# Kernel optimization log

Hardware: AMD Instinct MI355X
Metric: run time of the kernel (lower is better)

Reference implementation:

```python
import jax, jax.numpy as jnp
import numpy as np

DIM = 128
HEADS = 4
KV_RANK = 64
Q_RANK = 32
ROPE = DIM // 2   # 64
NOPE = DIM // 2   # 64
VDIM = DIM // 2   # 64
B, H, W = 2, 64, 64
EPS = 1e-5


def _conv1x1(x, w, b):
    # x: [B,C,H,W], w: [O,C], b: [O]
    return jnp.einsum('bchw,oc->bohw', x, w) + b[None, :, None, None]


def _gn1(x, g, b):
    # GroupNorm with 1 group: normalize over (C,H,W) per sample
    mu = jnp.mean(x, axis=(1, 2, 3), keepdims=True)
    var = jnp.mean((x - mu) ** 2, axis=(1, 2, 3), keepdims=True)
    return (x - mu) / jnp.sqrt(var + EPS) * g[None, :, None, None] + b[None, :, None, None]


def _freqs(h, w):
    # Replicates RotaryPositionalEncoding: pe[...,0::4]=sin_h, 1::4=cos_h, 2::4=sin_w, 3::4=cos_w
    n = ROPE // 4
    inv = 1.0 / (10000.0 ** (jnp.arange(n, dtype=jnp.float32) / n))
    ah = jnp.arange(h, dtype=jnp.float32)[:, None] * inv  # [h,n]
    aw = jnp.arange(w, dtype=jnp.float32)[:, None] * inv  # [w,n]
    fh = jnp.stack([jnp.sin(ah), jnp.cos(ah)], -1)  # [h,n,2] -> (real=sin_h, imag=cos_h)
    fw = jnp.stack([jnp.sin(aw), jnp.cos(aw)], -1)  # [w,n,2]
    fh_b = jnp.broadcast_to(fh[:, None], (h, w, n, 2))
    fw_b = jnp.broadcast_to(fw[None, :], (h, w, n, 2))
    # interleave pairs: pair 2m -> fh[m], pair 2m+1 -> fw[m]
    pe = jnp.stack([fh_b, fw_b], axis=3).reshape(h * w, ROPE // 2, 2)
    return pe  # [S, ROPE//2, 2]


def _rope(x, f):
    # x: [..., S, ROPE]; f: [S, ROPE//2, 2]
    xp = x.reshape(x.shape[:-1] + (ROPE // 2, 2))
    fr, fi = f[..., 0], f[..., 1]  # [S, ROPE//2] broadcast over leading dims
    rr = xp[..., 0] * fr - xp[..., 1] * fi
    ri = xp[..., 0] * fi + xp[..., 1] * fr
    return jnp.stack([rr, ri], -1).reshape(x.shape)


def setup_inputs() -> dict:
    key = jax.random.key(0)
    ks = jax.random.split(key, 8)
    s = 0.02
    inp = {
        'x': jax.random.normal(ks[0], (B, DIM, H, W), dtype=jnp.float32),
        'q1_w': jax.random.normal(ks[1], (Q_RANK, DIM), dtype=jnp.float32) * s,
        'q1_b': jnp.zeros((Q_RANK,), jnp.float32),
        'q_gn_g': jnp.ones((Q_RANK,), jnp.float32),
        'q_gn_b': jnp.zeros((Q_RANK,), jnp.float32),
        'q2_w': jax.random.normal(ks[2], (HEADS * (NOPE + ROPE), Q_RANK), dtype=jnp.float32) * s,
        'q2_b': jnp.zeros((HEADS * (NOPE + ROPE),), jnp.float32),
        'kv1_w': jax.random.normal(ks[3], (KV_RANK + ROPE, DIM), dtype=jnp.float32) * s,
        'kv1_b': jnp.zeros((KV_RANK + ROPE,), jnp.float32),
        'kv_gn_g': jnp.ones((KV_RANK + ROPE,), jnp.float32),
        'kv_gn_b': jnp.zeros((KV_RANK + ROPE,), jnp.float32),
        'kvn_g': jnp.ones((KV_RANK,), jnp.float32),
        'kvn_b': jnp.zeros((KV_RANK,), jnp.float32),
        'kvup_w': jax.random.normal(ks[4], (HEADS * (NOPE + VDIM), KV_RANK), dtype=jnp.float32) * s,
        'kvup_b': jnp.zeros((HEADS * (NOPE + VDIM),), jnp.float32),
        'out_w': jax.random.normal(ks[5], (DIM, HEADS * VDIM), dtype=jnp.float32) * s,
        'out_b': jnp.zeros((DIM,), jnp.float32),
    }
    return inp


def reference(x, q1_w, q1_b, q_gn_g, q_gn_b, q2_w, q2_b, kv1_w, kv1_b, kv_gn_g, kv_gn_b, kvn_g, kvn_b, kvup_w, kvup_b, out_w, out_b):
    b, c, h, w = x.shape
    s = h * w
    f = _freqs(h, w)  # [S, ROPE//2, 2]

    # Q path: low-rank down -> GN -> up
    q = _conv1x1(_gn1(_conv1x1(x, q1_w, q1_b), q_gn_g, q_gn_b), q2_w, q2_b)
    q = q.reshape(b, HEADS, NOPE + ROPE, s).transpose(0, 1, 3, 2)  # [B,H,S,D]
    q_nope, q_rope = q[..., :NOPE], q[..., NOPE:]
    q = jnp.concatenate([q_nope, _rope(q_rope, f)], axis=-1)

    # KV path: joint down-proj, split rope-k and compressed kv
    kv = _gn1(_conv1x1(x, kv1_w, kv1_b), kv_gn_g, kv_gn_b)  # [B, ROPE+KV_RANK, H, W]
    k_rope_c, kv_c = kv[:, :ROPE], kv[:, ROPE:]
    kv_u = _conv1x1(_gn1(kv_c, kvn_g, kvn_b), kvup_w, kvup_b)
    kv_u = kv_u.reshape(b, HEADS, NOPE + VDIM, s).transpose(0, 1, 3, 2)
    k_nope, v = kv_u[..., :NOPE], kv_u[..., NOPE:]

    k_rope = _rope(k_rope_c.reshape(b, ROPE, s).transpose(0, 2, 1)[:, None], f)  # [B,1,S,ROPE]
    k = jnp.concatenate([k_nope, jnp.broadcast_to(k_rope, (b, HEADS, s, ROPE))], axis=-1)

    scale = (NOPE + ROPE) ** -0.5
    attn = jax.nn.softmax(jnp.einsum('bhqd,bhkd->bhqk', q, k) * scale, axis=-1)
    o = jnp.einsum('bhqk,bhkd->bhqd', attn, v)  # [B,H,S,VDIM]
    o = o.transpose(0, 1, 3, 2).reshape(b, HEADS * VDIM, h, w)
    return _conv1x1(o, out_w, out_b) + x
```

## Files before the change

### kernel.cpp

```cpp
#include <hip/hip_runtime.h>

typedef unsigned short ushort_t;
typedef unsigned int uint_t;
typedef __attribute__((ext_vector_type(8))) short s16x8;
typedef __attribute__((ext_vector_type(4))) short s16x4;
typedef __attribute__((ext_vector_type(4))) float f32x4;
typedef __attribute__((ext_vector_type(16))) float f32x16;

#define S_TOT 4096
#define QSCALE 0.08838834764831845f
#define LOG2E 1.4426950408889634f
#define QSL (QSCALE * LOG2E)
#define L2_10000_D16 0.8304820237218406f

__device__ __forceinline__ ushort_t f2b(float f) {
  uint_t u = __float_as_uint(f);
  uint_t r = (u + 0x7FFFu + ((u >> 16) & 1u)) >> 16;
  return (ushort_t)r;
}

__device__ __forceinline__ float b2f(ushort_t u) {
  return __uint_as_float((uint_t)u << 16);
}

__device__ __forceinline__ uint_t cvt_pk_bf16(float lo, float hi) {
  uint_t r;
  asm("v_cvt_pk_bf16_f32 %0, %1, %2" : "=v"(r) : "v"(lo), "v"(hi));
  return r;
}

__device__ __forceinline__ void gload16(const void* g, void* l) {
  __builtin_amdgcn_global_load_lds(
      (const __attribute__((address_space(1))) unsigned int*)g,
      (__attribute__((address_space(3))) unsigned int*)l, 16, 0, 0);
}

__device__ __forceinline__ void rope_pair_t(float& x0, float& x1, int p, int hi, int wi,
                                            float scale, const float2* __restrict__ tab) {
  int j = p >> 1;
  int src = (p & 1) ? wi : hi;
  float2 sc = tab[src * 16 + j];
  float r0 = (x0 * sc.x - x1 * sc.y) * scale;
  float r1 = (x0 * sc.y + x1 * sc.x) * scale;
  x0 = r0; x1 = r1;
}

__global__ __launch_bounds__(256) void k_conv1(
    const float* __restrict__ x, const float* __restrict__ q1_w, const float* __restrict__ q1_b,
    const float* __restrict__ kv1_w, const float* __restrict__ kv1_b,
    float* __restrict__ y_q, float* __restrict__ y_kv, double* __restrict__ pch,
    const float* __restrict__ q2_w, const float* __restrict__ q2_b,
    const float* __restrict__ kvup_w, const float* __restrict__ kvup_b,
    const float* __restrict__ out_w, const float* __restrict__ out_b,
    ushort_t* __restrict__ wq2, ushort_t* __restrict__ wout,
    float* __restrict__ q2b2, float* __restrict__ outb2) {
  if (blockIdx.x >= 512) {
    int E = (blockIdx.x - 512) * 256 + threadIdx.x;
    if (E < 16384) {
      int oc = E >> 5, r = E & 31;
      int h = oc >> 7, d = oc & 127;
      float val;
      if (d < 64) {
        val = 0.f;
        for (int dd = 0; dd < 64; dd++)
          val += kvup_w[(h * 128 + dd) * 64 + d] * q2_w[(size_t)(h * 128 + dd) * 32 + r];
      } else {
        val = q2_w[(size_t)oc * 32 + r];
      }
      wq2[(size_t)oc * 32 + r] = f2b(val);
    } else if (E < 49152) {
      int e = E - 16384;
      int c = e >> 8, col = e & 255;
      int h = col >> 6, l = col & 63;
      float val = 0.f;
      for (int vd = 0; vd < 64; vd++)
        val += out_w[(size_t)c * 256 + h * 64 + vd] * kvup_w[(h * 128 + 64 + vd) * 64 + l];
      wout[(size_t)c * 256 + col] = f2b(val);
    } else if (E < 49664) {
      int oc = E - 49152;
      int h = oc >> 7, d = oc & 127;
      float val;
      if (d < 64) {
        val = 0.f;
        for (int dd = 0; dd < 64; dd++)
          val += kvup_w[(h * 128 + dd) * 64 + d] * q2_b[h * 128 + dd];
      } else val = q2_b[oc];
      q2b2[oc] = val;
    } else if (E < 49792) {
      int c = E - 49664;
      float val = out_b[c];
      for (int j = 0; j < 256; j++) {
        int h = j >> 6, vd = j & 63;
        val += out_w[(size_t)c * 256 + j] * kvup_b[h * 128 + 64 + vd];
      }
      outb2[c] = val;
    }
    return;
  }
  const int b = blockIdx.x >> 8, blk = blockIdx.x & 255, st = blk * 16;
  const int t = threadIdx.x, si = t & 15, g = t >> 4;
  __shared__ float xs[128][16];
#pragma unroll
  for (int i = 0; i < 8; i++) {
    int c = g + 16 * i;
    xs[c][si] = x[(size_t)(b * 128 + c) * S_TOT + st + si];
  }
  __syncthreads();
  float acc[10];
#pragma unroll
  for (int i = 0; i < 10; i++) {
    int oc = g * 10 + i;
    acc[i] = (oc < 32) ? q1_b[oc] : kv1_b[oc - 32];
  }
  const float4* q1w4 = (const float4*)q1_w;
  const float4* kv1w4 = (const float4*)kv1_w;
  for (int c4 = 0; c4 < 32; c4++) {
    float x0 = xs[c4 * 4 + 0][si], x1 = xs[c4 * 4 + 1][si];
    float x2 = xs[c4 * 4 + 2][si], x3 = xs[c4 * 4 + 3][si];
#pragma unroll
    for (int i = 0; i < 10; i++) {
      int oc = g * 10 + i;
      float4 wv = (oc < 32) ? q1w4[oc * 32 + c4] : kv1w4[(oc - 32) * 32 + c4];
      acc[i] += wv.x * x0 + wv.y * x1 + wv.z * x2 + wv.w * x3;
    }
  }
#pragma unroll
  for (int i = 0; i < 10; i++) {
    int oc = g * 10 + i;
    float a = acc[i];
    if (oc < 32) y_q[(size_t)(b * 32 + oc) * S_TOT + st + si] = a;
    else         y_kv[(size_t)(b * 128 + oc - 32) * S_TOT + st + si] = a;
    double s = a, q = (double)a * a;
#pragma unroll
    for (int o = 1; o < 16; o <<= 1) { s += __shfl_xor(s, o, 16); q += __shfl_xor(q, o, 16); }
    if (si == 0) {
      double* pt = pch + (size_t)(b * 160 + oc) * 512 + blk * 2;
      pt[0] = s; pt[1] = q;
    }
  }
}

__global__ __launch_bounds__(256) void k_red(
    const double* __restrict__ pch, double* __restrict__ SQ) {
  const int pair = blockIdx.x, tid = threadIdx.x;
  const int lane = tid & 63, wid = tid >> 6;
  const double* p = pch + (size_t)pair * 512;
  double s = p[tid * 2], q = p[tid * 2 + 1];
#pragma unroll
  for (int o = 1; o < 64; o <<= 1) { s += __shfl_xor(s, o, 64); q += __shfl_xor(q, o, 64); }
  __shared__ double red[4][2];
  if (lane == 0) { red[wid][0] = s; red[wid][1] = q; }
  __syncthreads();
  if (tid == 0) {
    SQ[pair * 2]     = red[0][0] + red[1][0] + red[2][0] + red[3][0];
    SQ[pair * 2 + 1] = red[0][1] + red[1][1] + red[2][1] + red[3][1];
  }
}

__global__ __launch_bounds__(512) void k_stats(
    const double* __restrict__ SQ,
    const float* __restrict__ qg, const float* __restrict__ qb,
    const float* __restrict__ kvg, const float* __restrict__ kvb,
    const float* __restrict__ kng, const float* __restrict__ knb,
    float* __restrict__ coef, float2* __restrict__ tab) {
  __shared__ double Sh[2][160], Qh[2][160];
  const int tid = threadIdx.x;
  for (int i = tid; i < 1024; i += 512) {
    int src = i >> 4, j = i & 15;
    float inv = exp2f(-(float)j * L2_10000_D16);
    float ang = (float)src * inv;
    tab[i] = make_float2(sinf(ang), cosf(ang));
  }
  if (tid < 320) {
    int b = tid / 160, c = tid % 160;
    Sh[b][c] = SQ[tid * 2]; Qh[b][c] = SQ[tid * 2 + 1];
  }
  __syncthreads();
  if (tid < 2) {
    int b = tid;
    float* cf = coef + b * 320;
    const double NS = 4096.0;
    double muq = 0, m2q = 0;
    for (int c = 0; c < 32; c++) { muq += Sh[b][c]; m2q += Qh[b][c]; }
    muq /= (32.0 * NS); m2q /= (32.0 * NS);
    double rstdq = 1.0 / sqrt(m2q - muq * muq + 1e-5);
    for (int c = 0; c < 32; c++) {
      double A = rstdq * (double)qg[c];
      cf[c] = (float)A; cf[32 + c] = (float)((double)qb[c] - muq * A);
    }
    double mukv = 0, m2kv = 0;
    for (int c = 0; c < 128; c++) { mukv += Sh[b][32 + c]; m2kv += Qh[b][32 + c]; }
    mukv /= (128.0 * NS); m2kv /= (128.0 * NS);
    double rstdkv = 1.0 / sqrt(m2kv - mukv * mukv + 1e-5);
    for (int c = 0; c < 64; c++) {
      double A = rstdkv * (double)kvg[c];
      cf[64 + c] = (float)A; cf[128 + c] = (float)((double)kvb[c] - mukv * A);
    }
    double mu2 = 0, m22 = 0;
    for (int c2 = 0; c2 < 64; c2++) {
      int c = 64 + c2;
      double a = rstdkv * (double)kvg[c], bb = (double)kvb[c] - mukv * a;
      double Ec = Sh[b][32 + c] / NS, M2c = Qh[b][32 + c] / NS;
      mu2 += a * Ec + bb;
      m22 += a * a * M2c + 2.0 * a * bb * Ec + bb * bb;
    }
    mu2 /= 64.0; m22 /= 64.0;
    double rstd2 = 1.0 / sqrt(m22 - mu2 * mu2 + 1e-5);
    for (int c2 = 0; c2 < 64; c2++) {
      int c = 64 + c2;
      double a = rstdkv * (double)kvg[c], bb = (double)kvb[c] - mukv * a;
      cf[192 + c2] = (float)(a * rstd2 * (double)kng[c2]);
      cf[256 + c2] = (float)((bb - mu2) * rstd2 * (double)kng[c2] + (double)knb[c2]);
    }
  }
}

__device__ __forceinline__ void gq_body(
    int id, ushort_t* smem,
    const float* __restrict__ y_q, const float* __restrict__ coef,
    const ushort_t* __restrict__ wq2, const float* __restrict__ q2b2,
    const float2* __restrict__ tab, ushort_t* __restrict__ Q) {
  const int h = id & 3, st = (id >> 2) & 63, b = id >> 8;
  const int t = threadIdx.x, si = t & 63, wid = t >> 6;
  const int l15 = t & 15, lg = (t >> 4) & 3;
  const float* cf = coef + b * 320;
  ushort_t* Xt = smem;
  ushort_t* sQ = smem + 4096;
  {
    ushort_t pk[8];
#pragma unroll
    for (int j = 0; j < 8; j++) {
      int c = wid * 8 + j;
      float v = y_q[(size_t)(b * 32 + c) * S_TOT + st * 64 + si];
      pk[j] = f2b(v * cf[c] + cf[32 + c]);
    }
    *(s16x8*)((char*)(Xt + si * 64) + ((wid * 16) ^ ((si & 7) << 4))) = *(s16x8*)pk;
  }
  __syncthreads();
  const int d0w = wid * 32;
  f32x4 acc[2][4];
#pragma unroll
  for (int db = 0; db < 2; db++) {
    f32x4 bv;
#pragma unroll
    for (int r = 0; r < 4; r++) bv[r] = q2b2[h * 128 + d0w + db * 16 + lg * 4 + r];
#pragma unroll
    for (int sb = 0; sb < 4; sb++) acc[db][sb] = bv;
  }
  s16x8 wf[2];
#pragma unroll
  for (int db = 0; db < 2; db++)
    wf[db] = *(const s16x8*)(wq2 + (size_t)(h * 128 + d0w + db * 16 + l15) * 32 + lg * 8);
  const int xsw = (lg * 16) ^ ((l15 & 7) << 4);
#pragma unroll
  for (int sb = 0; sb < 4; sb++) {
    s16x8 xf = *(const s16x8*)((const char*)(Xt + (sb * 16 + l15) * 64) + xsw);
#pragma unroll
    for (int db = 0; db < 2; db++)
      acc[db][sb] = __builtin_amdgcn_mfma_f32_16x16x32_bf16(wf[db], xf, acc[db][sb], 0, 0, 0);
  }
  if (wid >= 2) {
#pragma unroll
    for (int db = 0; db < 2; db++)
#pragma unroll
      for (int sb = 0; sb < 4; sb++) {
        int sp = st * 64 + sb * 16 + l15, hi = sp >> 6, wi = sp & 63;
        int dg = d0w + db * 16 + lg * 4;
#pragma unroll
        for (int pr = 0; pr < 2; pr++) {
          float v0 = acc[db][sb][pr * 2], v1 = acc[db][sb][pr * 2 + 1];
          int p = (dg + pr * 2 - 64) >> 1;
          rope_pair_t(v0, v1, p, hi, wi, QSL, tab);
          acc[db][sb][pr * 2] = v0; acc[db][sb][pr * 2 + 1] = v1;
        }
      }
  } else {
#pragma unroll
    for (int db = 0; db < 2; db++)
#pragma unroll
      for (int sb = 0; sb < 4; sb++)
#pragma unroll
        for (int r = 0; r < 4; r++) acc[db][sb][r] *= QSL;
  }
#pragma unroll
  for (int db = 0; db < 2; db++)
#pragma unroll
    for (int sb = 0; sb < 4; sb++) {
      ushort_t pk[4];
#pragma unroll
      for (int r = 0; r < 4; r++) pk[r] = f2b(acc[db][sb][r]);
      int srow = sb * 16 + l15;
      *(s16x4*)((char*)(sQ + srow * 128) + (((d0w + db * 16 + lg * 4) * 2) ^ ((srow & 7) << 4))) =
          *(s16x4*)pk;
    }
  __syncthreads();
  ushort_t* qrow = Q + ((size_t)(b * 4 + h) * S_TOT + st * 64 + si) * 128 + wid * 32;
#pragma unroll
  for (int j = 0; j < 4; j++) {
    s16x8 v = *(const s16x8*)((const char*)(sQ + si * 128) + ((wid * 64 + j * 16) ^ ((si & 7) << 4)));
    *(s16x8*)(qrow + j * 8) = v;
  }
}

__device__ __forceinline__ void lat_body(
    int blk, const float* __restrict__ y_kv, const float* __restrict__ coef,
    const float2* __restrict__ tab, ushort_t* __restrict__ C, ushort_t* __restrict__ VT) {
  const int b = blk >> 6, st = (blk & 63) * 64;
  const int t = threadIdx.x, si = t & 63, g = t >> 6;
  const float* cf = coef + b * 320;
  const int sp = st + si;
  if (g < 2) {
    const int c0 = g * 32;
    float v[32];
#pragma unroll
    for (int j = 0; j < 32; j++) {
      int c = c0 + j;
      v[j] = y_kv[(size_t)(b * 128 + c) * S_TOT + sp] * cf[64 + c] + cf[128 + c];
    }
    const int hi = sp >> 6, wi = sp & 63;
#pragma unroll
    for (int k = 0; k < 16; k++)
      rope_pair_t(v[2 * k], v[2 * k + 1], (c0 >> 1) + k, hi, wi, 1.0f, tab);
    ushort_t pk[32];
#pragma unroll
    for (int j = 0; j < 32; j++) pk[j] = f2b(v[j]);
    ushort_t* crow = C + (size_t)(b * S_TOT + sp) * 128 + 64 + c0;
#pragma unroll
    for (int j4 = 0; j4 < 4; j4++) *(s16x8*)(crow + j4 * 8) = *(s16x8*)(pk + j4 * 8);
  } else {
    const int c0 = (g - 2) * 32;
    ushort_t pk[32];
#pragma unroll
    for (int j = 0; j < 32; j++) {
      int c2 = c0 + j;
      float v = y_kv[(size_t)(b * 128 + 64 + c2) * S_TOT + sp] * cf[192 + c2] + cf[256 + c2];
      ushort_t u = f2b(v);
      pk[j] = u;
      VT[(size_t)(b * 64 + c2) * S_TOT + sp] = u;
    }
    ushort_t* crow = C + (size_t)(b * S_TOT + sp) * 128 + c0;
#pragma unroll
    for (int j4 = 0; j4 < 4; j4++) *(s16x8*)(crow + j4 * 8) = *(s16x8*)(pk + j4 * 8);
  }
}

__global__ __launch_bounds__(256) void k_build(
    const float* __restrict__ y_q, const float* __restrict__ y_kv,
    const float* __restrict__ coef,
    const ushort_t* __restrict__ wq2, const float* __restrict__ q2b2,
    const float2* __restrict__ tab,
    ushort_t* __restrict__ Q, ushort_t* __restrict__ C, ushort_t* __restrict__ VT) {
  __shared__ __align__(16) ushort_t smem[12288];
  if (blockIdx.x < 512) gq_body(blockIdx.x, smem, y_q, coef, wq2, q2b2, tab, Q);
  else                  lat_body(blockIdx.x - 512, y_kv, coef, tab, C, VT);
}

__global__ __launch_bounds__(256, 2) void k_attn(
    const ushort_t* __restrict__ Q, const ushort_t* __restrict__ C,
    const ushort_t* __restrict__ VT, ushort_t* __restrict__ Opart,
    float* __restrict__ lvec) {
  const int bid = blockIdx.x;
  const int bh = bid & 7;
  const int rest = bid >> 3;
  const int half = rest >> 5, qblk = rest & 31;
  const int kv0 = half * 2048;
  const int tid = threadIdx.x;
  const int wid = tid >> 6, lane = tid & 63;
  const int l31 = lane & 31, hi = lane >> 5;
  const int qbase = qblk * 128 + wid * 32;
  const int b4 = bh >> 2;
  const ushort_t* Qp = Q + (size_t)bh * S_TOT * 128;
  const ushort_t* Kp = C + (size_t)b4 * S_TOT * 128;
  const ushort_t* Vp = VT + (size_t)b4 * 64 * S_TOT;

  __shared__ __align__(16) ushort_t K_lds[3][64][128];
  __shared__ __align__(16) ushort_t V_lds[3][64][64];

  s16x8 qf[8];
#pragma unroll
  for (int c = 0; c < 8; c++)
    qf[c] = *(const s16x8*)(Qp + (size_t)(qbase + l31) * 128 + c * 16 + hi * 8);

  f32x16 o0, o1;
#pragma unroll
  for (int r = 0; r < 16; r++) { o0[r] = 0.f; o1[r] = 0.f; }
  float l_s = 0.f;

  const int krow_l = tid >> 4;
  const int kcolb = (tid & 15) * 16;
  const int vrow_l = tid >> 3;
  const int vcolb = (tid & 7) * 16;

#define STAGE(kvb, bufi)                                                          \
  {                                                                               \
    _Pragma("unroll")                                                             \
    for (int i = 0; i < 4; i++) {                                                 \
      int row = i * 16 + krow_l;                                                  \
      int colb = kcolb ^ ((row & 15) << 4);                                       \
      gload16((const char*)(Kp + (size_t)((kvb) + row) * 128) + colb,             \
              (void*)&K_lds[bufi][i * 16 + wid * 4][0]);                          \
    }                                                                             \
    _Pragma("unroll")                                                             \
    for (int i = 0; i < 2; i++) {                                                 \
      int vd = i * 32 + vrow_l;                                                   \
      int colb = vcolb ^ ((vd & 7) << 4);                                         \
      gload16((const char*)(Vp + (size_t)vd * S_TOT + (kvb)) + colb,              \
              (void*)&V_lds[bufi][i * 32 + wid * 8][0]);                          \
    }                                                                             \
  }

  STAGE(kv0, 0);
  STAGE(kv0 + 64, 1);

  const int kswz = (l31 & 15) << 4;
  const int vswz = (l31 & 7) << 4;
#pragma unroll 1
  for (int t = 0; t < 32; t++) {
    const int buf = t % 3;
    if (t < 31) {
      asm volatile("s_waitcnt vmcnt(6)" ::: "memory");
    } else {
      asm volatile("s_waitcnt vmcnt(0)" ::: "memory");
    }
    __builtin_amdgcn_sched_barrier(0);
    __builtin_amdgcn_s_barrier();
    __builtin_amdgcn_sched_barrier(0);
    if (t < 30) STAGE(kv0 + (t + 2) * 64, (t + 2) % 3);
    f32x16 sc0, sc1;
#pragma unroll
    for (int r = 0; r < 16; r++) { sc0[r] = 0.f; sc1[r] = 0.f; }
    __builtin_amdgcn_s_setprio(1);
#pragma unroll
    for (int c = 0; c < 8; c++) {
      const int off = (c * 32 + hi * 16) ^ kswz;
      s16x8 k0 = *(const s16x8*)((const char*)&K_lds[buf][l31][0] + off);
      s16x8 k1 = *(const s16x8*)((const char*)&K_lds[buf][32 + l31][0] + off);
      sc0 = __builtin_amdgcn_mfma_f32_32x32x16_bf16(k0, qf[c], sc0, 0, 0, 0);
      sc1 = __builtin_amdgcn_mfma_f32_32x32x16_bf16(k1, qf[c], sc1, 0, 0, 0);
    }
    __builtin_amdgcn_s_setprio(0);
    float rs = 0.f;
#pragma unroll
    for (int r = 0; r < 16; r++) {
      float p0 = exp2f(sc0[r]);
      float p1 = exp2f(sc1[r]);
      sc0[r] = p0; sc1[r] = p1;
      rs += p0 + p1;
    }
    l_s += rs;
    __builtin_amdgcn_s_setprio(1);
#pragma unroll
    for (int c = 0; c < 4; c++) {
      const f32x16 P = (c < 2) ? sc0 : sc1;
      const int rA = 8 * (c & 1);
      uint_t a0 = cvt_pk_bf16(P[rA + 0], P[rA + 1]);
      uint_t a1 = cvt_pk_bf16(P[rA + 2], P[rA + 3]);
      uint_t b0 = cvt_pk_bf16(P[rA + 4], P[rA + 5]);
      uint_t b1 = cvt_pk_bf16(P[rA + 6], P[rA + 7]);
      asm volatile("v_permlane32_swap_b32 %0, %1" : "+v"(a0), "+v"(b0));
      asm volatile("v_permlane32_swap_b32 %0, %1" : "+v"(a1), "+v"(b1));
      union { uint_t u[4]; s16x8 v; } pf;
      pf.u[0] = a0; pf.u[1] = a1;
      pf.u[2] = b0; pf.u[3] = b1;
      const int voff = (c * 32 + hi * 16) ^ vswz;
      s16x8 v0 = *(const s16x8*)((const char*)&V_lds[buf][l31][0] + voff);
      s16x8 v1 = *(const s16x8*)((const char*)&V_lds[buf][32 + l31][0] + voff);
      o0 = __builtin_amdgcn_mfma_f32_32x32x16_bf16(v0, pf.v, o0, 0, 0, 0);
      o1 = __builtin_amdgcn_mfma_f32_32x32x16_bf16(v1, pf.v, o1, 0, 0, 0);
    }
    __builtin_amdgcn_s_setprio(0);
  }
#undef STAGE
  l_s += __shfl_xor(l_s, 32, 64);
  if (lane < 32)
    lvec[((size_t)(half * 8 + bh) << 12) + qbase + l31] = l_s;
  char* sO = (char*)&K_lds[0][0][0];
#pragma unroll
  for (int vt = 0; vt < 2; vt++) {
#pragma unroll
    for (int r = 0; r < 16; r += 2) {
      float v0 = (vt ? o1[r] : o0[r]);
      float v1 = (vt ? o1[r + 1] : o0[r + 1]);
      uint_t u = cvt_pk_bf16(v0, v1);
      int vd = vt * 32 + (r & 3) + 8 * (r >> 2) + 4 * hi;
      *(uint_t*)(sO + (wid * 32 + l31) * 128 + ((vd * 2) ^ ((l31 & 7) << 4))) = u;
    }
  }
  __syncthreads();
  {
    const int r = tid >> 1, hf = tid & 1;
    const int w = r >> 5, ql = r & 31;
    ushort_t* orow = Opart + ((size_t)(half * 8 + bh) * S_TOT + qblk * 128 + r) * 64 + hf * 32;
#pragma unroll
    for (int j = 0; j < 4; j++) {
      s16x8 v = *(const s16x8*)(sO + (w * 32 + ql) * 128 + ((hf * 64 + j * 16) ^ ((ql & 7) << 4)));
      *(s16x8*)(orow + j * 8) = v;
    }
  }
}

__global__ __launch_bounds__(256) void k_oc(
    const ushort_t* __restrict__ Opart, const float* __restrict__ lvec,
    const ushort_t* __restrict__ wout, const float* __restrict__ outb2,
    const float* __restrict__ x, float* __restrict__ out) {
  const int id = blockIdx.x;
  const int cch = id & 1, st32 = (id >> 1) & 127, b = id >> 8;
  const int t = threadIdx.x, wid = t >> 6;
  const int l15 = t & 15, lg = (t >> 4) & 3;
  __shared__ __align__(16) ushort_t Xt[32][256];
  {
    const int s = t & 31, grp = t >> 5;
    const int h = grp >> 1, vd0 = (grp & 1) * 32;
    const int sp = st32 * 32 + s;
    const float l0 = lvec[((size_t)(b * 4 + h) << 12) + sp];
    const float l1 = lvec[((size_t)(8 + b * 4 + h) << 12) + sp];
    const float w = 1.f / (l0 + l1);
    const ushort_t* oa = Opart + ((size_t)(b * 4 + h) * S_TOT + sp) * 64 + vd0;
    const ushort_t* obp = oa + (size_t)8 * S_TOT * 64;
#pragma unroll
    for (int j4 = 0; j4 < 4; j4++) {
      union { s16x8 v; ushort_t u[8]; } av, bv2;
      av.v = *(const s16x8*)(oa + j4 * 8);
      bv2.v = *(const s16x8*)(obp + j4 * 8);
      ushort_t pk[8];
#pragma unroll
      for (int j = 0; j < 8; j++) pk[j] = f2b(w * (b2f(av.u[j]) + b2f(bv2.u[j])));
      *(s16x8*)((char*)&Xt[s][0] + ((grp * 64 + j4 * 16) ^ ((s & 7) << 4))) = *(s16x8*)pk;
    }
  }
  __syncthreads();
  const int c0w = cch * 64 + wid * 16;
  f32x4 acc[2];
  {
    f32x4 bv;
#pragma unroll
    for (int r = 0; r < 4; r++) bv[r] = outb2[c0w + lg * 4 + r];
    acc[0] = bv; acc[1] = bv;
  }
#pragma unroll
  for (int kk = 0; kk < 8; kk++) {
    s16x8 wf = *(const s16x8*)(wout + (size_t)(c0w + l15) * 256 + kk * 32 + lg * 8);
#pragma unroll
    for (int sb = 0; sb < 2; sb++) {
      s16x8 xf = *(const s16x8*)((const char*)&Xt[sb * 16 + l15][0] +
                                 ((kk * 64 + lg * 16) ^ ((l15 & 7) << 4)));
      acc[sb] = __builtin_amdgcn_mfma_f32_16x16x32_bf16(wf, xf, acc[sb], 0, 0, 0);
    }
  }
#pragma unroll
  for (int sb = 0; sb < 2; sb++) {
#pragma unroll
    for (int r = 0; r < 4; r++) {
      int c = c0w + lg * 4 + r;
      int sp = st32 * 32 + sb * 16 + l15;
      size_t idx = (size_t)(b * 128 + c) * S_TOT + sp;
      out[idx] = acc[sb][r] + x[idx];
    }
  }
}

extern "C" void kernel_launch(void* const* d_in, const int* in_sizes, int n_in,
                              void* d_out, int out_size, void* d_ws, size_t ws_size,
                              hipStream_t stream) {
  const float* x      = (const float*)d_in[0];
  const float* q1_w   = (const float*)d_in[1];
  const float* q1_b   = (const float*)d_in[2];
  const float* q_gn_g = (const float*)d_in[3];
  const float* q_gn_b = (const float*)d_in[4];
  const float* q2_w   = (const float*)d_in[5];
  const float* q2_b   = (const float*)d_in[6];
  const float* kv1_w  = (const float*)d_in[7];
  const float* kv1_b  = (const float*)d_in[8];
  const float* kv_gn_g= (const float*)d_in[9];
  const float* kv_gn_b= (const float*)d_in[10];
  const float* kvn_g  = (const float*)d_in[11];
  const float* kvn_b  = (const float*)d_in[12];
  const float* kvup_w = (const float*)d_in[13];
  const float* kvup_b = (const float*)d_in[14];
  const float* out_w  = (const float*)d_in[15];
  const float* out_b  = (const float*)d_in[16];

  const size_t MB = 1u << 20;
  char* ws = (char*)d_ws;
  float*    y_q   = (float*)(ws);
  float*    y_kv  = (float*)(ws + 1 * MB);
  ushort_t* Q     = (ushort_t*)(ws + 5 * MB);
  ushort_t* C     = (ushort_t*)(ws + 13 * MB);
  ushort_t* VT    = (ushort_t*)(ws + 15 * MB);
  double*   pch   = (double*)(ws + 17 * MB);
  double*   SQ    = (double*)(ws + 19 * MB);
  float*    coef  = (float*)(ws + 19 * MB + 8192);
  ushort_t* wq2   = (ushort_t*)(ws + 19 * MB + 16384);
  ushort_t* wout  = (ushort_t*)(ws + 19 * MB + 65536);
  float*    q2b2  = (float*)(ws + 19 * MB + 131072);
  float*    outb2 = (float*)(ws + 19 * MB + 139264);
  float2*   tab   = (float2*)(ws + 19 * MB + 143360);
  ushort_t* Opart = (ushort_t*)(ws + 20 * MB);
  float*    lvec  = (float*)(ws + 28 * MB);
  float*    out   = (float*)d_out;

  k_conv1<<<707, 256, 0, stream>>>(x, q1_w, q1_b, kv1_w, kv1_b, y_q, y_kv, pch,
                                   q2_w, q2_b, kvup_w, kvup_b, out_w, out_b,
                                   wq2, wout, q2b2, outb2);
  k_red  <<<320, 256, 0, stream>>>(pch, SQ);
  k_stats<<<1,   512, 0, stream>>>(SQ, q_gn_g, q_gn_b, kv_gn_g, kv_gn_b, kvn_g, kvn_b,
                                   coef, tab);
  k_build<<<640, 256, 0, stream>>>(y_q, y_kv, coef, wq2, q2b2, tab, Q, C, VT);
  k_attn <<<512, 256, 0, stream>>>(Q, C, VT, Opart, lvec);
  k_oc   <<<512, 256, 0, stream>>>(Opart, lvec, wout, outb2, x, out);
}
```

Measured before the change: 143.3 us.

## Compute first 1x1 conv with bf16 MFMA and move GN stats to reduction kernel

The first projection (x to q-down and kv-down channels) now runs on bf16 MFMA 16x16x32 instructions, using a swizzled LDS tile of x converted to bf16, with 32 spatial positions per block instead of a scalar fp32 FMA loop. The per-block double-precision partial sums for GroupNorm are dropped from the conv kernel, and k_red now reads the full y_q/y_kv rows directly to compute sum and sum of squares. This shortens the conv kernel and removes the partial-sum buffer, but it rereads the conv output in k_red and lowers the first-projection precision to bf16 inputs.

```diff
diff --git a/kernel.cpp b/kernel.cpp
--- a/kernel.cpp
+++ b/kernel.cpp
@@ -48,14 +48,14 @@
 __global__ __launch_bounds__(256) void k_conv1(
     const float* __restrict__ x, const float* __restrict__ q1_w, const float* __restrict__ q1_b,
     const float* __restrict__ kv1_w, const float* __restrict__ kv1_b,
-    float* __restrict__ y_q, float* __restrict__ y_kv, double* __restrict__ pch,
+    float* __restrict__ y_q, float* __restrict__ y_kv,
     const float* __restrict__ q2_w, const float* __restrict__ q2_b,
     const float* __restrict__ kvup_w, const float* __restrict__ kvup_b,
     const float* __restrict__ out_w, const float* __restrict__ out_b,
     ushort_t* __restrict__ wq2, ushort_t* __restrict__ wout,
     float* __restrict__ q2b2, float* __restrict__ outb2) {
-  if (blockIdx.x >= 512) {
-    int E = (blockIdx.x - 512) * 256 + threadIdx.x;
+  if (blockIdx.x >= 256) {
+    int E = (blockIdx.x - 256) * 256 + threadIdx.x;
     if (E < 16384) {
       int oc = E >> 5, r = E & 31;
       int h = oc >> 7, d = oc & 127;
@@ -97,55 +97,78 @@
     }
     return;
   }
-  const int b = blockIdx.x >> 8, blk = blockIdx.x & 255, st = blk * 16;
-  const int t = threadIdx.x, si = t & 15, g = t >> 4;
-  __shared__ float xs[128][16];
-#pragma unroll
-  for (int i = 0; i < 8; i++) {
-    int c = g + 16 * i;
-    xs[c][si] = x[(size_t)(b * 128 + c) * S_TOT + st + si];
+  const int id = blockIdx.x;
+  const int b = id >> 7, blk = id & 127, st = blk * 32;
+  const int t = threadIdx.x, wid = t >> 6;
+  const int l15 = t & 15, lg = (t >> 4) & 3;
+  __shared__ __align__(16) ushort_t Xt[32][128];
+  {
+    const int si = t & 31, g = t >> 5;
+#pragma unroll
+    for (int half = 0; half < 2; half++) {
+      ushort_t pk[8];
+#pragma unroll
+      for (int j = 0; j < 8; j++) {
+        int c = g * 16 + half * 8 + j;
+        pk[j] = f2b(x[(size_t)(b * 128 + c) * S_TOT + st + si]);
+      }
+      *(s16x8*)((char*)&Xt[si][0] + ((g * 32 + half * 16) ^ ((si & 15) << 4))) = *(s16x8*)pk;
+    }
   }
   __syncthreads();
-  float acc[10];
-#pragma unroll
-  for (int i = 0; i < 10; i++) {
-    int oc = g * 10 + i;
-    acc[i] = (oc < 32) ? q1_b[oc] : kv1_b[oc - 32];
-  }
-  const float4* q1w4 = (const float4*)q1_w;
-  const float4* kv1w4 = (const float4*)kv1_w;
-  for (int c4 = 0; c4 < 32; c4++) {
-    float x0 = xs[c4 * 4 + 0][si], x1 = xs[c4 * 4 + 1][si];
-    float x2 = xs[c4 * 4 + 2][si], x3 = xs[c4 * 4 + 3][si];
-#pragma unroll
-    for (int i = 0; i < 10; i++) {
-      int oc = g * 10 + i;
-      float4 wv = (oc < 32) ? q1w4[oc * 32 + c4] : kv1w4[(oc - 32) * 32 + c4];
-      acc[i] += wv.x * x0 + wv.y * x1 + wv.z * x2 + wv.w * x3;
-    }
-  }
-#pragma unroll
-  for (int i = 0; i < 10; i++) {
-    int oc = g * 10 + i;
-    float a = acc[i];
-    if (oc < 32) y_q[(size_t)(b * 32 + oc) * S_TOT + st + si] = a;
-    else         y_kv[(size_t)(b * 128 + oc - 32) * S_TOT + st + si] = a;
-    double s = a, q = (double)a * a;
-#pragma unroll
-    for (int o = 1; o < 16; o <<= 1) { s += __shfl_xor(s, o, 16); q += __shfl_xor(q, o, 16); }
-    if (si == 0) {
-      double* pt = pch + (size_t)(b * 160 + oc) * 512 + blk * 2;
-      pt[0] = s; pt[1] = q;
+#pragma unroll
+  for (int k5 = 0; k5 < 5; k5++) {
+    const int tt = wid * 5 + k5;
+    const int rt = tt >> 1, ct = tt & 1;
+    const int oc0 = rt * 16;
+    f32x4 acc;
+#pragma unroll
+    for (int r = 0; r < 4; r++) {
+      int oc = oc0 + lg * 4 + r;
+      acc[r] = (oc < 32) ? q1_b[oc] : kv1_b[oc - 32];
+    }
+    const int wrow = oc0 + l15;
+    const float4* wr4 = (wrow < 32) ? ((const float4*)q1_w) + (size_t)wrow * 32
+                                    : ((const float4*)kv1_w) + (size_t)(wrow - 32) * 32;
+    const int xrow = ct * 16 + l15;
+    const int xswz = (xrow & 15) << 4;
+#pragma unroll
+    for (int kk = 0; kk < 4; kk++) {
+      float4 wa = wr4[kk * 8 + lg * 2];
+      float4 wb = wr4[kk * 8 + lg * 2 + 1];
+      ushort_t wp[8];
+      wp[0] = f2b(wa.x); wp[1] = f2b(wa.y); wp[2] = f2b(wa.z); wp[3] = f2b(wa.w);
+      wp[4] = f2b(wb.x); wp[5] = f2b(wb.y); wp[6] = f2b(wb.z); wp[7] = f2b(wb.w);
+      s16x8 wf = *(s16x8*)wp;
+      s16x8 xf = *(const s16x8*)((const char*)&Xt[xrow][0] + ((kk * 64 + lg * 16) ^ xswz));
+      acc = __builtin_amdgcn_mfma_f32_16x16x32_bf16(wf, xf, acc, 0, 0, 0);
+    }
+    const int sp = st + ct * 16 + l15;
+#pragma unroll
+    for (int r = 0; r < 4; r++) {
+      int oc = oc0 + lg * 4 + r;
+      if (oc < 32) y_q[(size_t)(b * 32 + oc) * S_TOT + sp] = acc[r];
+      else         y_kv[(size_t)(b * 128 + oc - 32) * S_TOT + sp] = acc[r];
     }
   }
 }
 
 __global__ __launch_bounds__(256) void k_red(
-    const double* __restrict__ pch, double* __restrict__ SQ) {
+    const float* __restrict__ y_q, const float* __restrict__ y_kv,
+    double* __restrict__ SQ) {
   const int pair = blockIdx.x, tid = threadIdx.x;
   const int lane = tid & 63, wid = tid >> 6;
-  const double* p = pch + (size_t)pair * 512;
-  double s = p[tid * 2], q = p[tid * 2 + 1];
+  const int b = pair / 160, c = pair % 160;
+  const float* row = (c < 32) ? y_q + ((size_t)(b * 32 + c) << 12)
+                              : y_kv + ((size_t)(b * 128 + c - 32) << 12);
+  const float4* r4 = (const float4*)row;
+  double s = 0, q = 0;
+#pragma unroll
+  for (int j = 0; j < 4; j++) {
+    float4 v = r4[tid * 4 + j];
+    s += (double)v.x + (double)v.y + (double)v.z + (double)v.w;
+    q += (double)v.x * v.x + (double)v.y * v.y + (double)v.z * v.z + (double)v.w * v.w;
+  }
 #pragma unroll
   for (int o = 1; o < 64; o <<= 1) { s += __shfl_xor(s, o, 64); q += __shfl_xor(q, o, 64); }
   __shared__ double red[4][2];
@@ -587,7 +610,6 @@
   ushort_t* Q     = (ushort_t*)(ws + 5 * MB);
   ushort_t* C     = (ushort_t*)(ws + 13 * MB);
   ushort_t* VT    = (ushort_t*)(ws + 15 * MB);
-  double*   pch   = (double*)(ws + 17 * MB);
   double*   SQ    = (double*)(ws + 19 * MB);
   float*    coef  = (float*)(ws + 19 * MB + 8192);
   ushort_t* wq2   = (ushort_t*)(ws + 19 * MB + 16384);
@@ -599,10 +621,10 @@
   float*    lvec  = (float*)(ws + 28 * MB);
   float*    out   = (float*)d_out;
 
-  k_conv1<<<707, 256, 0, stream>>>(x, q1_w, q1_b, kv1_w, kv1_b, y_q, y_kv, pch,
+  k_conv1<<<451, 256, 0, stream>>>(x, q1_w, q1_b, kv1_w, kv1_b, y_q, y_kv,
                                    q2_w, q2_b, kvup_w, kvup_b, out_w, out_b,
                                    wq2, wout, q2b2, outb2);
-  k_red  <<<320, 256, 0, stream>>>(pch, SQ);
+  k_red  <<<320, 256, 0, stream>>>(y_q, y_kv, SQ);
   k_stats<<<1,   512, 0, stream>>>(SQ, q_gn_g, q_gn_b, kv_gn_g, kv_gn_b, kvn_g, kvn_b,
                                    coef, tab);
   k_build<<<640, 256, 0, stream>>>(y_q, y_kv, coef, wq2, q2b2, tab, Q, C, VT);
```

Measured after the change: 126.2 us. 1.14x faster.
